# Kernel optimization log

Measured on AMD Instinct MI355X. Metric: run time of the kernel, lower is better.

## Reference

```python
import jax, jax.numpy as jnp
import numpy as np

SIGMA = 1.0
DELTA = 1.0
TOPK = 10
TOPK_HALF = 5  # int(np.around(TOPK / 2))
N, D = 4096, 512
N_IDS = 2048  # N / view


def _l2_normalize(x, eps=1e-12):
    n = jnp.linalg.norm(x, axis=1, keepdims=True)
    return x / jnp.maximum(n, eps)


def _cdist(a, b):
    # Euclidean distance with a sqrt that is safe at 0 (diagonal).
    sq = (jnp.sum(a * a, 1)[:, None] + jnp.sum(b * b, 1)[None, :]
          - 2.0 * (a @ b.T))
    sq = jnp.maximum(sq, 0.0)
    return jnp.where(sq > 0, jnp.sqrt(jnp.where(sq > 0, sq, 1.0)), 0.0)


def setup_inputs() -> dict:
    key = jax.random.key(0)
    k1, k2, k3 = jax.random.split(key, 3)
    s_emb = jax.random.normal(k1, (N, D), dtype=jnp.float32)
    t_emb = jax.random.normal(k2, (N, D), dtype=jnp.float32)
    idx = jax.random.randint(k3, (N,), 0, N_IDS, dtype=jnp.int64)
    return {"s_emb": s_emb, "t_emb": t_emb, "idx": idx}


def reference(s_emb, t_emb, idx):
    n = s_emb.shape[0]
    s = _l2_normalize(s_emb)          # disable_mu=True
    t = _l2_normalize(t_emb)

    S_dist = _cdist(s, s)
    S_dist = S_dist / jnp.mean(S_dist, axis=1, keepdims=True)

    # --- teacher-side neighbor graph (no_grad in original) ---
    T_dist = _cdist(t, t)
    W_P = jnp.exp(-(T_dist ** 2) / SIGMA)                      # [N,N]
    same = idx[:, None] == idx[None, :]
    W_P_copy = jnp.where(same, 1.0, W_P)
    _, topk_index = jax.lax.top_k(W_P_copy, TOPK)              # [N,k]
    topk_half_index = topk_index[:, :TOPK_HALF]                # [N,k/2]

    rows = jnp.arange(n)[:, None]
    W_NN = jnp.zeros((n, n), jnp.float32).at[rows, topk_index].set(1.0)
    V = ((W_NN + W_NN.T) / 2.0 == 1.0).astype(jnp.float32)     # mutual kNN

    # Vectorized form of the per-row nonzero gather-reduce loop:
    # W_C_tilda[i,j] = V[i,j] * (sum_l V[i,l] V[j,l]) / |{l: V[i,l]>0}|
    row_cnt = jnp.sum(V, axis=1)                               # [N]
    VV = jnp.einsum('il,jl->ij', V, V)                         # [N,N]
    W_C_tilda = jnp.where(V > 0, VV / jnp.maximum(row_cnt, 1.0)[:, None], 0.0)

    W_C_hat = jnp.mean(W_C_tilda[topk_half_index], axis=1)     # [N,k/2,N]->[N,N]
    W_C = (W_C_hat + W_C_hat.T) / 2.0
    W = (W_P + W_C) / 2.0

    eye = jnp.eye(n, dtype=jnp.float32)
    pos_weight = W * (1.0 - eye)
    neg_weight = (1.0 - W) * (1.0 - eye)

    pull = jnp.maximum(S_dist, 0.0) ** 2 * pos_weight
    push = jnp.maximum(DELTA - S_dist, 0.0) ** 2 * neg_weight
    loss = (jnp.sum(pull) + jnp.sum(push)) / (n * (n - 1))
    return loss
```

## Files before the change

kernel.cpp:

```cpp
#include <hip/hip_runtime.h>
#include <math.h>

#define N 4096
#define D 512
#define TOPK 10
#define TOPK_HALF 5
#define NT 32
#define TRI_BLOCKS (NT * (NT + 1) / 2)
#define WC_BLOCKS (N * TOPK_HALF / 16)
#define INV_N (1.0f / 4096.0f)
#define TPAD 132

typedef __bf16 bf16;
typedef __bf16 bf16x8 __attribute__((ext_vector_type(8)));
typedef float f32x4 __attribute__((ext_vector_type(4)));
typedef _Float16 f16;
typedef _Float16 f16x4 __attribute__((ext_vector_type(4)));
typedef _Float16 f16x8 __attribute__((ext_vector_type(8)));
typedef unsigned short u16;
typedef unsigned short u16x8 __attribute__((ext_vector_type(8)));
typedef unsigned int u32;

__device__ __forceinline__ void gl_lds16(const void* g, void* l) {
  __builtin_amdgcn_global_load_lds(
      (const __attribute__((address_space(1))) void*)g,
      (__attribute__((address_space(3))) void*)l, 16, 0, 0);
}

__device__ __forceinline__ float f16tof(u16 h) {
  return (float)__builtin_bit_cast(_Float16, h);
}

__global__ __launch_bounds__(256) void k_normalize2(const float* __restrict__ xs,
                                                    const float* __restrict__ xt,
                                                    bf16* __restrict__ ys,
                                                    bf16* __restrict__ yt,
                                                    float* __restrict__ rsq_s,
                                                    float* __restrict__ rsq_t,
                                                    float* __restrict__ rowsum) {
  int b = blockIdx.x;
  int row = b & (N - 1);
  int is_t = b >> 12;
  const float* x = is_t ? xt : xs;
  bf16* y = is_t ? yt : ys;
  float* rowsq = is_t ? rsq_t : rsq_s;
  int tid = threadIdx.x;
  const float* xr = x + (size_t)row * D;
  float v0 = xr[tid], v1 = xr[tid + 256];
  float ss = v0 * v0 + v1 * v1;
  __shared__ float red[4];
  for (int off = 32; off > 0; off >>= 1) ss += __shfl_down(ss, off, 64);
  if ((tid & 63) == 0) red[tid >> 6] = ss;
  __syncthreads();
  float tot = red[0] + red[1] + red[2] + red[3];
  float inv = 1.0f / fmaxf(sqrtf(tot), 1e-12f);
  bf16 b0 = (bf16)(v0 * inv), b1 = (bf16)(v1 * inv);
  bf16* yr = y + (size_t)row * D;
  yr[tid] = b0; yr[tid + 256] = b1;
  float f0 = (float)b0, f1 = (float)b1;
  float s2 = f0 * f0 + f1 * f1;
  for (int off = 32; off > 0; off >>= 1) s2 += __shfl_down(s2, off, 64);
  __syncthreads();
  if ((tid & 63) == 0) red[tid >> 6] = s2;
  __syncthreads();
  if (tid == 0) {
    rowsq[row] = red[0] + red[1] + red[2] + red[3];
    if (!is_t) rowsum[row] = 0.f;
  }
}

__global__ __launch_bounds__(256) void k_dgram3(const bf16* __restrict__ S,
                                                const bf16* __restrict__ T,
                                                const float* __restrict__ rsq_s,
                                                const float* __restrict__ rsq_t,
                                                f16* __restrict__ Gsd,
                                                f16* __restrict__ Gwp,
                                                float* __restrict__ rowsum) {
  __shared__ __align__(16) char sm[128 * TPAD * 2];
  bf16* Jb0 = (bf16*)sm;
  bf16* Jb1 = (bf16*)(sm + 8192);
  bf16* Ib0 = (bf16*)(sm + 16384);
  bf16* Ib1 = (bf16*)(sm + 24576);
  f16* tp = (f16*)sm;

  int z = blockIdx.y;
  const bf16* Y = z ? T : S;
  const float* rsq = z ? rsq_t : rsq_s;
  f16* G = z ? Gwp : Gsd;

  int t = blockIdx.x, by = 0;
  while (t >= NT - by) { t -= NT - by; ++by; }
  int bx = by + t;
  bool offdiag = (bx != by);

  int tid = threadIdx.x;
  int lane = tid & 63, w = tid >> 6;
  int wr = w >> 1, wc = w & 1;
  int quad = lane >> 4, c = lane & 15;

  const char* Jbase = (const char*)(Y + (size_t)(bx * 128) * D);
  const char* Ibase = (const char*)(Y + (size_t)(by * 128) * D);
  int r0 = tid >> 2, q0 = tid & 3;
  int r1 = (tid + 256) >> 2, q1 = (tid + 256) & 3;
  size_t so0 = (size_t)r0 * (D * 2) + q0 * 16;
  size_t so1 = (size_t)r1 * (D * 2) + q1 * 16;
  bf16* lJ0a = Jb0 + (size_t)w * 512;  bf16* lJ0b = Jb0 + (size_t)(256 + w * 64) * 8;
  bf16* lJ1a = Jb1 + (size_t)w * 512;  bf16* lJ1b = Jb1 + (size_t)(256 + w * 64) * 8;
  bf16* lI0a = Ib0 + (size_t)w * 512;  bf16* lI0b = Ib0 + (size_t)(256 + w * 64) * 8;
  bf16* lI1a = Ib1 + (size_t)w * 512;  bf16* lI1b = Ib1 + (size_t)(256 + w * 64) * 8;

  int jrow = wr * 64 + c;
  int irow = wc * 64 + c;
  int kq = quad * 8;

  f32x4 acc[4][4] = {};
  for (int k0 = 0; k0 < D; k0 += 64) {
    size_t kb = (size_t)k0 * 2;
    gl_lds16(Jbase + so0 + kb,      lJ0a);
    gl_lds16(Jbase + so1 + kb,      lJ0b);
    gl_lds16(Jbase + so0 + kb + 64, lJ1a);
    gl_lds16(Jbase + so1 + kb + 64, lJ1b);
    gl_lds16(Ibase + so0 + kb,      lI0a);
    gl_lds16(Ibase + so1 + kb,      lI0b);
    gl_lds16(Ibase + so0 + kb + 64, lI1a);
    gl_lds16(Ibase + so1 + kb + 64, lI1b);
    __syncthreads();
    {
      bf16x8 af[4], bfr[4];
#pragma unroll
      for (int u = 0; u < 4; ++u) af[u] = *(bf16x8*)&Jb0[(jrow + u * 16) * 32 + kq];
#pragma unroll
      for (int v = 0; v < 4; ++v) bfr[v] = *(bf16x8*)&Ib0[(irow + v * 16) * 32 + kq];
#pragma unroll
      for (int u = 0; u < 4; ++u)
#pragma unroll
        for (int v = 0; v < 4; ++v)
          acc[u][v] = __builtin_amdgcn_mfma_f32_16x16x32_bf16(af[u], bfr[v], acc[u][v], 0, 0, 0);
    }
    {
      bf16x8 af[4], bfr[4];
#pragma unroll
      for (int u = 0; u < 4; ++u) af[u] = *(bf16x8*)&Jb1[(jrow + u * 16) * 32 + kq];
#pragma unroll
      for (int v = 0; v < 4; ++v) bfr[v] = *(bf16x8*)&Ib1[(irow + v * 16) * 32 + kq];
#pragma unroll
      for (int u = 0; u < 4; ++u)
#pragma unroll
        for (int v = 0; v < 4; ++v)
          acc[u][v] = __builtin_amdgcn_mfma_f32_16x16x32_bf16(af[u], bfr[v], acc[u][v], 0, 0, 0);
    }
    __syncthreads();
  }

#pragma unroll
  for (int v = 0; v < 4; ++v) {
    int il = wc * 64 + v * 16 + c;
    int ig = by * 128 + il;
    float ri = rsq[ig];
    float rsv = 0.f;
#pragma unroll
    for (int u = 0; u < 4; ++u) {
      int jl0 = wr * 64 + u * 16 + quad * 4;
      int jb0i = bx * 128 + jl0;
      float4 rj = *(const float4*)(rsq + jb0i);
      const float* rjp = (const float*)&rj;
      f32x4 a = acc[u][v];
      f16x4 st;
      if (z == 0) {
#pragma unroll
        for (int reg = 0; reg < 4; ++reg) {
          float sq = fmaxf(ri + rjp[reg] - 2.0f * a[reg], 0.0f);
          float val = sqrtf(sq);
          st[reg] = (_Float16)val;
          rsv += val;
        }
      } else {
#pragma unroll
        for (int reg = 0; reg < 4; ++reg) {
          float sq = fmaxf(ri + rjp[reg] - 2.0f * a[reg], 0.0f);
          st[reg] = (_Float16)expf(-sq);
        }
      }
      *(f16x4*)(G + (size_t)ig * N + jb0i) = st;
      if (offdiag) {
#pragma unroll
        for (int reg = 0; reg < 4; ++reg) tp[(jl0 + reg) * TPAD + il] = st[reg];
      }
    }
    if (z == 0) {
      rsv += __shfl_xor(rsv, 16, 64);
      rsv += __shfl_xor(rsv, 32, 64);
      if (lane < 16) atomicAdd(&rowsum[ig], rsv);
    }
  }

  if (offdiag) {
    __syncthreads();
    int rloc = tid >> 4;
    int cseg = tid & 15;
#pragma unroll
    for (int it = 0; it < 8; ++it) {
      int jl = it * 16 + rloc;
      int jg = bx * 128 + jl;
      f16x8 v8 = *(f16x8*)&tp[jl * TPAD + cseg * 8];
      *(f16x8*)(G + (size_t)jg * N + by * 128 + cseg * 8) = v8;
      if (z == 0) {
        float csum = 0.f;
#pragma unroll
        for (int e = 0; e < 8; ++e) csum += (float)v8[e];
        csum += __shfl_xor(csum, 1, 64);
        csum += __shfl_xor(csum, 2, 64);
        csum += __shfl_xor(csum, 4, 64);
        csum += __shfl_xor(csum, 8, 64);
        if (cseg == 0) atomicAdd(&rowsum[jg], csum);
      }
    }
  }
}

__global__ __launch_bounds__(256) void k_rowpass(const f16* __restrict__ Gs,
                                                 const f16* __restrict__ Gw,
                                                 const int* __restrict__ ids,
                                                 const float* __restrict__ rowsum,
                                                 int* __restrict__ topk,
                                                 double* __restrict__ pd) {
  __shared__ u32 lds[256 * TOPK];
  __shared__ double dred[4];
  int i = blockIdx.x, tid = threadIdx.x;
  int idi = ids[i];
  float invm = 1.0f / (rowsum[i] * INV_N);
  const u16* srow = (const u16*)(Gs + (size_t)i * N);
  const u16* wrow = (const u16*)(Gw + (size_t)i * N);
  u32 key[16];
  float dsum = 0.f;
  int j0 = tid * 16;
#pragma unroll
  for (int h = 0; h < 2; ++h) {
    int jb = j0 + h * 8;
    u16x8 sv = *(const u16x8*)(srow + jb);
    u16x8 wv = *(const u16x8*)(wrow + jb);
    int4 id0 = *(const int4*)(ids + jb);
    int4 id1 = *(const int4*)(ids + jb + 4);
    const int* idp = (const int*)&id0;
    const int* idp1 = (const int*)&id1;
#pragma unroll
    for (int e = 0; e < 8; ++e) {
      int j = jb + e;
      u16 hw = wv[e];
      float wp = f16tof(hw);
      if (j != i) {
        float sdn = f16tof(sv[e]) * invm;
        float r = fmaxf(1.0f - sdn, 0.0f); r *= r;
        dsum += r + 0.5f * wp * (sdn * sdn - r);
      }
      int idj = (e < 4) ? idp[e] : idp1[e - 4];
      u16 hk = (idj == idi) ? (u16)0x3C00 : hw;
      key[h * 8 + e] = ((u32)hk << 16) | (u32)(4095 - j);
    }
  }
#pragma unroll
  for (int kk = 2; kk <= 16; kk <<= 1) {
#pragma unroll
    for (int jj = kk >> 1; jj > 0; jj >>= 1) {
#pragma unroll
      for (int ii = 0; ii < 16; ++ii) {
        int ll = ii ^ jj;
        if (ll > ii) {
          bool desc = ((ii & kk) == 0);
          u32 a = key[ii], b = key[ll];
          bool sw = desc ? (a < b) : (a > b);
          key[ii] = sw ? b : a;
          key[ll] = sw ? a : b;
        }
      }
    }
  }
  double dl = (double)dsum;
  for (int off = 32; off > 0; off >>= 1) dl += __shfl_down(dl, off, 64);
  if ((tid & 63) == 0) dred[tid >> 6] = dl;
#pragma unroll
  for (int o = 0; o < TOPK; ++o) lds[tid * TOPK + o] = key[o];
  __syncthreads();
  for (int off = 128; off >= 1; off >>= 1) {
    if (tid < off) {
      u32 A[TOPK], B[TOPK];
#pragma unroll
      for (int o = 0; o < TOPK; ++o) {
        A[o] = lds[tid * TOPK + o];
        B[o] = lds[(tid + off) * TOPK + o];
      }
      u32 out[TOPK];
#pragma unroll
      for (int o = 0; o < TOPK; ++o) {
        u32 m = A[o] > B[o] ? A[o] : B[o];
#pragma unroll
        for (int p = 0; p < o; ++p) {
          u32 mn = A[p] < B[o - 1 - p] ? A[p] : B[o - 1 - p];
          m = m > mn ? m : mn;
        }
        out[o] = m;
      }
#pragma unroll
      for (int o = 0; o < TOPK; ++o) lds[tid * TOPK + o] = out[o];
    }
    __syncthreads();
  }
  if (tid == 0) {
#pragma unroll
    for (int o = 0; o < TOPK; ++o)
      topk[i * TOPK + o] = 4095 - (int)(lds[o] & 0xFFFu);
    pd[i] = dred[0] + dred[1] + dred[2] + dred[3];
  }
}

__global__ __launch_bounds__(64) void k_buildV(const int* __restrict__ topk,
                                               int* __restrict__ L,
                                               int* __restrict__ cnt) {
  int i = blockIdx.x * 64 + threadIdx.x;
  if (i >= N) return;
  int c = 0;
  for (int r = 0; r < TOPK; ++r) {
    int j = topk[i * TOPK + r];
    bool mut = false;
    for (int q = 0; q < TOPK; ++q) mut |= (topk[j * TOPK + q] == i);
    if (mut) L[i * TOPK + c++] = j;
  }
  cnt[i] = c;
}

__global__ __launch_bounds__(256) void k_wc(const int* __restrict__ topk,
                                            const int* __restrict__ L,
                                            const int* __restrict__ cnt,
                                            const f16* __restrict__ Gsd,
                                            const float* __restrict__ rowsum,
                                            double* __restrict__ pw) {
  __shared__ double red[16];
  int tid = threadIdx.x;
  int grp = tid >> 4;
  int gl = tid & 15;
  int task = blockIdx.x * 16 + grp;
  int i = task / TOPK_HALF, m = task % TOPK_HALF;
  int r = topk[i * TOPK + m];
  int cr = cnt[r];
  float invmi = 1.0f / (rowsum[i] * INV_N);
  int lval = (gl < cr) ? L[r * TOPK + gl] : -1;
  int Lr[TOPK];
#pragma unroll
  for (int a = 0; a < TOPK; ++a) Lr[a] = __shfl(lval, a, 16);
  float contrib = 0.f;
  if (gl < cr) {
    int j = lval;
    if (j != i) {
      int cj = cnt[j];
      float mj = rowsum[j] * INV_N;
      float sr_ = f16tof(((const u16*)Gsd)[(size_t)i * N + j]);
      int lj[TOPK];
#pragma unroll
      for (int b = 0; b < TOPK; ++b) lj[b] = L[j * TOPK + b];
      int vv = 0;
#pragma unroll
      for (int b = 0; b < TOPK; ++b) {
        if (b < cj) {
#pragma unroll
          for (int a = 0; a < TOPK; ++a)
            vv += ((a < cr) && (lj[b] == Lr[a])) ? 1 : 0;
        }
      }
      float denom = (float)(cr > 1 ? cr : 1);
      float wgt = (float)vv / denom;
      float sdij = sr_ * invmi;
      float sdji = sr_ / mj;
      float Rij = fmaxf(1.0f - sdij, 0.0f); Rij *= Rij;
      float Rji = fmaxf(1.0f - sdji, 0.0f); Rji *= Rji;
      float Fij = sdij * sdij - Rij;
      float Fji = sdji * sdji - Rji;
      contrib = wgt * (Fij + Fji);
    }
  }
  double local = (double)contrib;
  local += __shfl_xor(local, 1, 16);
  local += __shfl_xor(local, 2, 16);
  local += __shfl_xor(local, 4, 16);
  local += __shfl_xor(local, 8, 16);
  if (gl == 0) red[grp] = local;
  __syncthreads();
  if (tid == 0) {
    double s = 0.0;
#pragma unroll
    for (int g = 0; g < 16; ++g) s += red[g];
    pw[blockIdx.x] = s * (1.0 / 20.0);
  }
}

__global__ __launch_bounds__(256) void k_final(const double* __restrict__ pd,
                                               const double* __restrict__ pw,
                                               float* __restrict__ out) {
  int tid = threadIdx.x;
  double s = 0.0;
  for (int i = tid; i < N; i += 256) s += pd[i];
  for (int i = tid; i < WC_BLOCKS; i += 256) s += pw[i];
  for (int off = 32; off > 0; off >>= 1) s += __shfl_down(s, off, 64);
  __shared__ double red[4];
  if ((tid & 63) == 0) red[tid >> 6] = s;
  __syncthreads();
  if (tid == 0)
    out[0] = (float)((red[0] + red[1] + red[2] + red[3]) /
                     ((double)N * (double)(N - 1)));
}

extern "C" void kernel_launch(void* const* d_in, const int* in_sizes, int n_in,
                              void* d_out, int out_size, void* d_ws, size_t ws_size,
                              hipStream_t stream) {
  const float* s_emb = (const float*)d_in[0];
  const float* t_emb = (const float*)d_in[1];
  const int* ids = (const int*)d_in[2];
  float* out = (float*)d_out;

  char* ws = (char*)d_ws;
  size_t off = 0;
  bf16* snorm = (bf16*)(ws + off); off += (size_t)N * D * 2;
  bf16* tnorm = (bf16*)(ws + off); off += (size_t)N * D * 2;
  f16*  Gsd   = (f16*)(ws + off);  off += (size_t)N * N * 2;
  f16*  Gwp   = (f16*)(ws + off);  off += (size_t)N * N * 2;
  float* rsq_s = (float*)(ws + off); off += (size_t)N * 4;
  float* rsq_t = (float*)(ws + off); off += (size_t)N * 4;
  float* rowsum= (float*)(ws + off); off += (size_t)N * 4;
  int*   topk  = (int*)(ws + off);   off += (size_t)N * TOPK * 4;
  int*   L     = (int*)(ws + off);   off += (size_t)N * TOPK * 4;
  int*   cnt   = (int*)(ws + off);   off += (size_t)N * 4;
  off = (off + 15) & ~(size_t)15;
  double* pd   = (double*)(ws + off); off += (size_t)N * 8;
  double* pw   = (double*)(ws + off); off += (size_t)WC_BLOCKS * 8;

  k_normalize2<<<2 * N, 256, 0, stream>>>(s_emb, t_emb, snorm, tnorm,
                                          rsq_s, rsq_t, rowsum);
  k_dgram3<<<dim3(TRI_BLOCKS, 2), 256, 0, stream>>>(snorm, tnorm, rsq_s, rsq_t,
                                                    Gsd, Gwp, rowsum);
  k_rowpass<<<N, 256, 0, stream>>>(Gsd, Gwp, ids, rowsum, topk, pd);
  k_buildV<<<N / 64, 64, 0, stream>>>(topk, L, cnt);
  k_wc<<<WC_BLOCKS, 256, 0, stream>>>(topk, L, cnt, Gsd, rowsum, pw);
  k_final<<<1, 256, 0, stream>>>(pd, pw, out);
}
```

Before: 164.5 us.

## Split row top-k pass into half-row blocks and merge candidates in buildV

The row pass now handles each row as two 128-thread blocks, each covering half the columns. Each block writes a partial top-10 candidate list, which k_buildV merges per row, and it re-merges each neighbor's lists for the mutual-kNN test. This shortens the serial LDS tree reduction by one level and doubles the number of blocks. Separately, normalization now uses one wavefront per row with float4 loads and no shared-memory barriers. The cost is redundant candidate merging in buildV, which it does for every neighbor lookup.

```diff
diff --git a/kernel.cpp b/kernel.cpp
--- a/kernel.cpp
+++ b/kernel.cpp
@@ -12,6 +12,7 @@
 #define TPAD 132
 
 typedef __bf16 bf16;
+typedef __bf16 bf16x4 __attribute__((ext_vector_type(4)));
 typedef __bf16 bf16x8 __attribute__((ext_vector_type(8)));
 typedef float f32x4 __attribute__((ext_vector_type(4)));
 typedef _Float16 f16;
@@ -31,41 +32,55 @@
   return (float)__builtin_bit_cast(_Float16, h);
 }
 
-__global__ __launch_bounds__(256) void k_normalize2(const float* __restrict__ xs,
+__device__ __forceinline__ void merge10(const u32* A, const u32* B, u32* out) {
+#pragma unroll
+  for (int o = 0; o < TOPK; ++o) {
+    u32 m = A[o] > B[o] ? A[o] : B[o];
+#pragma unroll
+    for (int p = 0; p < o; ++p) {
+      u32 mn = A[p] < B[o - 1 - p] ? A[p] : B[o - 1 - p];
+      m = m > mn ? m : mn;
+    }
+    out[o] = m;
+  }
+}
+
+__global__ __launch_bounds__(256) void k_normalize3(const float* __restrict__ xs,
                                                     const float* __restrict__ xt,
                                                     bf16* __restrict__ ys,
                                                     bf16* __restrict__ yt,
                                                     float* __restrict__ rsq_s,
                                                     float* __restrict__ rsq_t,
                                                     float* __restrict__ rowsum) {
-  int b = blockIdx.x;
-  int row = b & (N - 1);
-  int is_t = b >> 12;
+  int w = threadIdx.x >> 6, l = threadIdx.x & 63;
+  int rg = blockIdx.x * 4 + w;
+  int is_t = rg >> 12;
+  int row = rg & (N - 1);
   const float* x = is_t ? xt : xs;
   bf16* y = is_t ? yt : ys;
-  float* rowsq = is_t ? rsq_t : rsq_s;
-  int tid = threadIdx.x;
   const float* xr = x + (size_t)row * D;
-  float v0 = xr[tid], v1 = xr[tid + 256];
-  float ss = v0 * v0 + v1 * v1;
-  __shared__ float red[4];
-  for (int off = 32; off > 0; off >>= 1) ss += __shfl_down(ss, off, 64);
-  if ((tid & 63) == 0) red[tid >> 6] = ss;
-  __syncthreads();
-  float tot = red[0] + red[1] + red[2] + red[3];
-  float inv = 1.0f / fmaxf(sqrtf(tot), 1e-12f);
-  bf16 b0 = (bf16)(v0 * inv), b1 = (bf16)(v1 * inv);
-  bf16* yr = y + (size_t)row * D;
-  yr[tid] = b0; yr[tid + 256] = b1;
-  float f0 = (float)b0, f1 = (float)b1;
-  float s2 = f0 * f0 + f1 * f1;
-  for (int off = 32; off > 0; off >>= 1) s2 += __shfl_down(s2, off, 64);
-  __syncthreads();
-  if ((tid & 63) == 0) red[tid >> 6] = s2;
-  __syncthreads();
-  if (tid == 0) {
-    rowsq[row] = red[0] + red[1] + red[2] + red[3];
-    if (!is_t) rowsum[row] = 0.f;
+  float4 a = *(const float4*)(xr + l * 4);
+  float4 b = *(const float4*)(xr + 256 + l * 4);
+  float ss = a.x * a.x + a.y * a.y + a.z * a.z + a.w * a.w +
+             b.x * b.x + b.y * b.y + b.z * b.z + b.w * b.w;
+#pragma unroll
+  for (int off = 32; off > 0; off >>= 1) ss += __shfl_xor(ss, off, 64);
+  float inv = 1.0f / fmaxf(sqrtf(ss), 1e-12f);
+  bf16x4 oa = {(bf16)(a.x * inv), (bf16)(a.y * inv), (bf16)(a.z * inv), (bf16)(a.w * inv)};
+  bf16x4 ob = {(bf16)(b.x * inv), (bf16)(b.y * inv), (bf16)(b.z * inv), (bf16)(b.w * inv)};
+  *(bf16x4*)(y + (size_t)row * D + l * 4) = oa;
+  *(bf16x4*)(y + (size_t)row * D + 256 + l * 4) = ob;
+  float s2 = 0.f;
+#pragma unroll
+  for (int e = 0; e < 4; ++e) {
+    float fa = (float)oa[e], fb = (float)ob[e];
+    s2 += fa * fa + fb * fb;
+  }
+#pragma unroll
+  for (int off = 32; off > 0; off >>= 1) s2 += __shfl_xor(s2, off, 64);
+  if (l == 0) {
+    if (is_t) rsq_t[row] = s2;
+    else { rsq_s[row] = s2; rowsum[row] = 0.f; }
   }
 }
 
@@ -218,19 +233,22 @@
   }
 }
 
-__global__ __launch_bounds__(256) void k_rowpass(const f16* __restrict__ Gs,
+__global__ __launch_bounds__(128) void k_rowpass(const f16* __restrict__ Gs,
                                                  const f16* __restrict__ Gw,
                                                  const int* __restrict__ ids,
                                                  const float* __restrict__ rowsum,
-                                                 int* __restrict__ topk,
+                                                 u32* __restrict__ cand2,
                                                  double* __restrict__ pd) {
-  __shared__ u32 lds[256 * TOPK];
-  __shared__ double dred[4];
-  int i = blockIdx.x, tid = threadIdx.x;
+  __shared__ u32 lds[128 * TOPK];
+  __shared__ double dred[2];
+  int b = blockIdx.x;
+  int i = b >> 1, half = b & 1;
+  int base = half * 2048;
+  int tid = threadIdx.x;
   int idi = ids[i];
   float invm = 1.0f / (rowsum[i] * INV_N);
-  const u16* srow = (const u16*)(Gs + (size_t)i * N);
-  const u16* wrow = (const u16*)(Gw + (size_t)i * N);
+  const u16* srow = (const u16*)(Gs + (size_t)i * N + base);
+  const u16* wrow = (const u16*)(Gw + (size_t)i * N + base);
   u32 key[16];
   float dsum = 0.f;
   int j0 = tid * 16;
@@ -239,23 +257,23 @@
     int jb = j0 + h * 8;
     u16x8 sv = *(const u16x8*)(srow + jb);
     u16x8 wv = *(const u16x8*)(wrow + jb);
-    int4 id0 = *(const int4*)(ids + jb);
-    int4 id1 = *(const int4*)(ids + jb + 4);
+    int4 id0 = *(const int4*)(ids + base + jb);
+    int4 id1 = *(const int4*)(ids + base + jb + 4);
     const int* idp = (const int*)&id0;
     const int* idp1 = (const int*)&id1;
 #pragma unroll
     for (int e = 0; e < 8; ++e) {
-      int j = jb + e;
+      int jg = base + jb + e;
       u16 hw = wv[e];
       float wp = f16tof(hw);
-      if (j != i) {
+      if (jg != i) {
         float sdn = f16tof(sv[e]) * invm;
         float r = fmaxf(1.0f - sdn, 0.0f); r *= r;
         dsum += r + 0.5f * wp * (sdn * sdn - r);
       }
       int idj = (e < 4) ? idp[e] : idp1[e - 4];
       u16 hk = (idj == idi) ? (u16)0x3C00 : hw;
-      key[h * 8 + e] = ((u32)hk << 16) | (u32)(4095 - j);
+      key[h * 8 + e] = ((u32)hk << 16) | (u32)(4095 - jg);
     }
   }
 #pragma unroll
@@ -267,10 +285,10 @@
         int ll = ii ^ jj;
         if (ll > ii) {
           bool desc = ((ii & kk) == 0);
-          u32 a = key[ii], b = key[ll];
-          bool sw = desc ? (a < b) : (a > b);
-          key[ii] = sw ? b : a;
-          key[ll] = sw ? a : b;
+          u32 a = key[ii], bb = key[ll];
+          bool sw = desc ? (a < bb) : (a > bb);
+          key[ii] = sw ? bb : a;
+          key[ll] = sw ? a : bb;
         }
       }
     }
@@ -281,25 +299,15 @@
 #pragma unroll
   for (int o = 0; o < TOPK; ++o) lds[tid * TOPK + o] = key[o];
   __syncthreads();
-  for (int off = 128; off >= 1; off >>= 1) {
+  for (int off = 64; off >= 1; off >>= 1) {
     if (tid < off) {
-      u32 A[TOPK], B[TOPK];
+      u32 A[TOPK], B[TOPK], out[TOPK];
 #pragma unroll
       for (int o = 0; o < TOPK; ++o) {
         A[o] = lds[tid * TOPK + o];
         B[o] = lds[(tid + off) * TOPK + o];
       }
-      u32 out[TOPK];
-#pragma unroll
-      for (int o = 0; o < TOPK; ++o) {
-        u32 m = A[o] > B[o] ? A[o] : B[o];
-#pragma unroll
-        for (int p = 0; p < o; ++p) {
-          u32 mn = A[p] < B[o - 1 - p] ? A[p] : B[o - 1 - p];
-          m = m > mn ? m : mn;
-        }
-        out[o] = m;
-      }
+      merge10(A, B, out);
 #pragma unroll
       for (int o = 0; o < TOPK; ++o) lds[tid * TOPK + o] = out[o];
     }
@@ -307,22 +315,43 @@
   }
   if (tid == 0) {
 #pragma unroll
-    for (int o = 0; o < TOPK; ++o)
-      topk[i * TOPK + o] = 4095 - (int)(lds[o] & 0xFFFu);
-    pd[i] = dred[0] + dred[1] + dred[2] + dred[3];
-  }
-}
-
-__global__ __launch_bounds__(64) void k_buildV(const int* __restrict__ topk,
+    for (int o = 0; o < TOPK; ++o) cand2[(size_t)b * TOPK + o] = lds[o];
+    pd[b] = dred[0] + dred[1];
+  }
+}
+
+__global__ __launch_bounds__(64) void k_buildV(const u32* __restrict__ cand2,
+                                               int* __restrict__ topk,
                                                int* __restrict__ L,
                                                int* __restrict__ cnt) {
   int i = blockIdx.x * 64 + threadIdx.x;
   if (i >= N) return;
+  u32 A[TOPK], B[TOPK], my[TOPK];
+#pragma unroll
+  for (int o = 0; o < TOPK; ++o) {
+    A[o] = cand2[(size_t)(i * 2) * TOPK + o];
+    B[o] = cand2[(size_t)(i * 2 + 1) * TOPK + o];
+  }
+  merge10(A, B, my);
+  int tk[TOPK];
+#pragma unroll
+  for (int o = 0; o < TOPK; ++o) {
+    tk[o] = 4095 - (int)(my[o] & 0xFFFu);
+    topk[i * TOPK + o] = tk[o];
+  }
   int c = 0;
   for (int r = 0; r < TOPK; ++r) {
-    int j = topk[i * TOPK + r];
+    int j = tk[r];
+    u32 JA[TOPK], JB[TOPK], jt[TOPK];
+#pragma unroll
+    for (int o = 0; o < TOPK; ++o) {
+      JA[o] = cand2[(size_t)(j * 2) * TOPK + o];
+      JB[o] = cand2[(size_t)(j * 2 + 1) * TOPK + o];
+    }
+    merge10(JA, JB, jt);
     bool mut = false;
-    for (int q = 0; q < TOPK; ++q) mut |= (topk[j * TOPK + q] == i);
+#pragma unroll
+    for (int q = 0; q < TOPK; ++q) mut |= ((4095 - (int)(jt[q] & 0xFFFu)) == i);
     if (mut) L[i * TOPK + c++] = j;
   }
   cnt[i] = c;
@@ -397,7 +426,7 @@
                                                float* __restrict__ out) {
   int tid = threadIdx.x;
   double s = 0.0;
-  for (int i = tid; i < N; i += 256) s += pd[i];
+  for (int i = tid; i < 2 * N; i += 256) s += pd[i];
   for (int i = tid; i < WC_BLOCKS; i += 256) s += pw[i];
   for (int off = 32; off > 0; off >>= 1) s += __shfl_down(s, off, 64);
   __shared__ double red[4];
@@ -429,15 +458,16 @@
   int*   L     = (int*)(ws + off);   off += (size_t)N * TOPK * 4;
   int*   cnt   = (int*)(ws + off);   off += (size_t)N * 4;
   off = (off + 15) & ~(size_t)15;
-  double* pd   = (double*)(ws + off); off += (size_t)N * 8;
+  u32*  cand2  = (u32*)(ws + off);   off += (size_t)N * 2 * TOPK * 4;
+  double* pd   = (double*)(ws + off); off += (size_t)N * 2 * 8;
   double* pw   = (double*)(ws + off); off += (size_t)WC_BLOCKS * 8;
 
-  k_normalize2<<<2 * N, 256, 0, stream>>>(s_emb, t_emb, snorm, tnorm,
-                                          rsq_s, rsq_t, rowsum);
+  k_normalize3<<<2048, 256, 0, stream>>>(s_emb, t_emb, snorm, tnorm,
+                                         rsq_s, rsq_t, rowsum);
   k_dgram3<<<dim3(TRI_BLOCKS, 2), 256, 0, stream>>>(snorm, tnorm, rsq_s, rsq_t,
                                                     Gsd, Gwp, rowsum);
-  k_rowpass<<<N, 256, 0, stream>>>(Gsd, Gwp, ids, rowsum, topk, pd);
-  k_buildV<<<N / 64, 64, 0, stream>>>(topk, L, cnt);
+  k_rowpass<<<2 * N, 128, 0, stream>>>(Gsd, Gwp, ids, rowsum, cand2, pd);
+  k_buildV<<<N / 64, 64, 0, stream>>>(cand2, topk, L, cnt);
   k_wc<<<WC_BLOCKS, 256, 0, stream>>>(topk, L, cnt, Gsd, rowsum, pw);
   k_final<<<1, 256, 0, stream>>>(pd, pw, out);
 }
```

Measured after the change: 171.5 us. 1.04x slower.
